# Kernel tuning notes

Measured on AMD Instinct MI355X. Metric: run time of the kernel, lower is better.

The kernel has to match this reference:

```python
import jax, jax.numpy as jnp
import numpy as np


def setup_inputs() -> dict:
    key = jax.random.key(0)
    ks = jax.random.split(key, 7)
    B, S, D = 256, 1024, 128  # batch of sets, set size, n_input
    H = 256
    x = jax.random.normal(ks[0], (B, S, D), dtype=jnp.float32)
    # torch nn.Linear weights: [out_features, in_features], in = 2*layer_in
    W0 = jax.random.normal(ks[1], (H, 2 * D), dtype=jnp.float32) * 0.05
    b0 = jnp.zeros((H,), dtype=jnp.float32)
    W1 = jax.random.normal(ks[2], (H, 2 * H), dtype=jnp.float32) * 0.05
    b1 = jnp.zeros((H,), dtype=jnp.float32)
    W2 = jax.random.normal(ks[3], (H, 2 * H), dtype=jnp.float32) * 0.05
    b2 = jnp.zeros((H,), dtype=jnp.float32)
    return {"x": x, "W0": W0, "b0": b0, "W1": W1, "b1": b1, "W2": W2, "b2": b2}


def reference(x, W0, b0, W1, b1, W2, b2):
    # x: [B, S, D] batch of sets. Original loops over batch; we vmap.
    def apply_set(y):
        # y: [S, d]
        for W, b in ((W0, b0), (W1, b1), (W2, b2)):
            mean = jnp.mean(y, axis=0, keepdims=True)            # [1, d]
            mean = jnp.broadcast_to(mean, y.shape)               # [S, d]
            z = jnp.concatenate([y, mean], axis=1)               # [S, 2d]
            y = jnp.tanh(z @ W.T + b)                            # [S, out]
        return jnp.mean(y, axis=0)                               # [out]
    return jax.vmap(apply_set)(x)                                # [B, out]
```

## Files before the change

### kernel.cpp

```cpp
#include <hip/hip_runtime.h>

#define B_ 256
#define S_ 1024
#define D_ 128
#define H_ 256

typedef short short8 __attribute__((ext_vector_type(8)));
typedef float f32x4 __attribute__((ext_vector_type(4)));

__device__ unsigned short g_Wb0[H_ * D_];
__device__ unsigned short g_Wb1[H_ * H_];
__device__ unsigned short g_Wb2[H_ * H_];
__device__ float g_Wc0[H_ * D_];
__device__ float g_Wc1[H_ * H_];
__device__ float g_Wc2[H_ * H_];
__device__ float g_mean0[B_ * D_];
__device__ float g_colsum1[B_ * H_];
__device__ float g_colsum2[B_ * H_];
__device__ float g_c0[B_ * H_];
__device__ float g_c1[B_ * H_];
__device__ float g_c2[B_ * H_];
__device__ unsigned short g_xb[(size_t)B_ * S_ * D_];

__device__ __forceinline__ unsigned short f2bf(float x) {
    union { float f; unsigned u; } v; v.f = x;
    unsigned r = v.u + 0x7FFFu + ((v.u >> 16) & 1u);
    return (unsigned short)(r >> 16);
}
__device__ __forceinline__ float bf2f(unsigned short h) {
    union { float f; unsigned u; } v; v.u = ((unsigned)h) << 16;
    return v.f;
}
__device__ __forceinline__ float fast_tanh(float x) {
    float e = __builtin_amdgcn_exp2f(x * 2.885390081777927f);
    float r = __builtin_amdgcn_rcpf(1.0f + e);
    return 1.0f - 2.0f * r;
}
__device__ __forceinline__ unsigned cvt_pk_bf16(float lo, float hi) {
    unsigned r;
    asm("v_cvt_pk_bf16_f32 %0, %1, %2" : "=v"(r) : "v"(lo), "v"(hi));
    return r;
}
__device__ __forceinline__ void gload_lds16(const unsigned short* g, unsigned short* l) {
    __builtin_amdgcn_global_load_lds(
        (const __attribute__((address_space(1))) void*)g,
        (__attribute__((address_space(3))) void*)l, 16, 0, 0);
}
__device__ __forceinline__ float row16_reduce_add(float v) {
    int s;
    s = __builtin_amdgcn_update_dpp(0, __builtin_bit_cast(int, v), 0x111, 0xF, 0xF, true);
    v += __builtin_bit_cast(float, s);
    s = __builtin_amdgcn_update_dpp(0, __builtin_bit_cast(int, v), 0x112, 0xF, 0xF, true);
    v += __builtin_bit_cast(float, s);
    s = __builtin_amdgcn_update_dpp(0, __builtin_bit_cast(int, v), 0x114, 0xF, 0xF, true);
    v += __builtin_bit_cast(float, s);
    s = __builtin_amdgcn_update_dpp(0, __builtin_bit_cast(int, v), 0x118, 0xF, 0xF, true);
    v += __builtin_bit_cast(float, s);
    return v;
}

__global__ __launch_bounds__(256) void prep_kernel(
    const float* __restrict__ W0, const float* __restrict__ W1,
    const float* __restrict__ W2)
{
    int i = blockIdx.x * 256 + threadIdx.x;
    const float* W; unsigned short* wb; float* wc; int kbits;
    if (i < H_ * D_) { W = W0; wb = g_Wb0; wc = g_Wc0; kbits = 7; }
    else {
        i -= H_ * D_;
        if (i < H_ * H_) { W = W1; wb = g_Wb1; wc = g_Wc1; kbits = 8; }
        else {
            i -= H_ * H_;
            if (i >= H_ * H_) return;
            W = W2; wb = g_Wb2; wc = g_Wc2; kbits = 8;
        }
    }
    const int K = 1 << kbits, KS = K >> 5;
    const int n = i >> kbits, k = i & (K - 1);
    const float a = W[n * 2 * K + k];
    const float b = W[n * 2 * K + K + k];
    const unsigned short hb = f2bf(a);
    const int w = n >> 5, cf = (n >> 4) & 1, l15 = n & 15;
    const int ks = k >> 5, quad = (k >> 3) & 3, e = k & 7;
    wb[(((w * 2 + cf) * KS + ks) * 64 + quad * 16 + l15) * 8 + e] = hb;
    wc[n * K + k] = b + (a - bf2f(hb));
}

__global__ __launch_bounds__(1024) void means0_kernel(const float* __restrict__ x)
{
    const int set = blockIdx.x, t = threadIdx.x;
    const int cg = t & 31, rg = t >> 5;
    const float* xs = x + (size_t)set * S_ * D_;
    unsigned short* xd = g_xb + (size_t)set * S_ * D_;
    const int slot = cg >> 1, halfsel = (cg & 1) * 4;
    f32x4 s = (f32x4){0.f, 0.f, 0.f, 0.f};
    #pragma unroll 8
    for (int i = 0; i < 32; ++i) {
        const int row = rg + i * 32;
        f32x4 v = *(const f32x4*)(xs + row * D_ + cg * 4);
        s += v;
        uint2 pv;
        pv.x = cvt_pk_bf16(v[0], v[1]);
        pv.y = cvt_pk_bf16(v[2], v[3]);
        *(uint2*)(&xd[row * D_ + ((slot ^ (row & 7)) * 8) + halfsel]) = pv;
    }
    __shared__ f32x4 red[32][32];
    red[rg][cg] = s;
    __syncthreads();
    if (t < 32) {
        f32x4 a = red[0][t];
        #pragma unroll
        for (int g = 1; g < 32; ++g) a += red[g][t];
        #pragma unroll
        for (int c = 0; c < 4; ++c) g_mean0[set * D_ + t * 4 + c] = a[c];
    }
}

template <int L>
__global__ __launch_bounds__(256) void c_kernel(const float* __restrict__ bias)
{
    constexpr int K = (L == 0) ? D_ : H_;
    constexpr int KB = (L == 0) ? 7 : 8;
    const int j = threadIdx.x, sg = blockIdx.x * 4;
    const float* Wc = (L == 0) ? g_Wc0 : (L == 1) ? g_Wc1 : g_Wc2;
    const float* ms = (L == 0) ? g_mean0 : (L == 1) ? g_colsum1 : g_colsum2;
    float* dst = (L == 0) ? g_c0 : (L == 1) ? g_c1 : g_c2;
    __shared__ float m_lds[4][H_];
    for (int i = j; i < 4 * K; i += 256)
        m_lds[i >> KB][i & (K - 1)] = ms[(sg + (i >> KB)) * K + (i & (K - 1))] * (1.f / S_);
    __syncthreads();
    const float* wr = Wc + j * K;
    float a0 = 0.f, a1 = 0.f, a2 = 0.f, a3 = 0.f;
    #pragma unroll 4
    for (int k = 0; k < K; k += 4) {
        f32x4 w = *(const f32x4*)(wr + k);
        #pragma unroll
        for (int c = 0; c < 4; ++c) {
            a0 += m_lds[0][k + c] * w[c];
            a1 += m_lds[1][k + c] * w[c];
            a2 += m_lds[2][k + c] * w[c];
            a3 += m_lds[3][k + c] * w[c];
        }
    }
    const float bb = bias[j];
    dst[(sg + 0) * H_ + j] = bb + a0;
    dst[(sg + 1) * H_ + j] = bb + a1;
    dst[(sg + 2) * H_ + j] = bb + a2;
    dst[(sg + 3) * H_ + j] = bb + a3;
}

template <int LAYER>
__global__ __launch_bounds__(512, 2) void layer_kernel(
    unsigned short* ybuf, float* __restrict__ out)
{
    constexpr int K  = (LAYER == 0) ? D_ : H_;
    constexpr int KS = K / 32;
    constexpr int NCH = (64 * K / 8) / 512;
    constexpr int NT = S_ / 64;
    const int set = blockIdx.x;
    const int t = threadIdx.x;
    const int lane = t & 63, wave = t >> 6;
    const int l15 = lane & 15, quad = lane >> 4;

    __shared__ __align__(16) unsigned short y_lds[2][64 * K];

    const unsigned short* Wb = (LAYER == 0) ? g_Wb0 : (LAYER == 1) ? g_Wb1 : g_Wb2;
    const float* cvec = (LAYER == 0) ? g_c0 : (LAYER == 1) ? g_c1 : g_c2;
    const unsigned short* ysrc = (LAYER == 0) ? g_xb + (size_t)set * S_ * D_
                                              : ybuf + (size_t)set * S_ * H_;
    unsigned short* ydst = ybuf + (size_t)set * S_ * H_;

    short8 wf[2][KS];
    {
        const unsigned short* wb = Wb + (wave * 2 * KS * 64 + lane) * 8;
        #pragma unroll
        for (int cf = 0; cf < 2; ++cf)
            #pragma unroll
            for (int ks = 0; ks < KS; ++ks)
                wf[cf][ks] = *(const short8*)(wb + (cf * KS + ks) * 512);
    }
    const float* cv = cvec + set * H_ + wave * 32 + quad * 4;
    f32x4 creg0 = *(const f32x4*)(cv);
    f32x4 creg1 = *(const f32x4*)(cv + 16);

    #pragma unroll
    for (int c = 0; c < NCH; ++c)
        gload_lds16(ysrc + (c * 512 + t) * 8, &y_lds[0][(c * 512 + t) * 8]);

    f32x4 cs0 = (f32x4){0.f, 0.f, 0.f, 0.f};
    f32x4 cs1 = (f32x4){0.f, 0.f, 0.f, 0.f};
    __syncthreads();

    for (int tt = 0; tt < NT; ++tt) {
        const int buf = tt & 1;
        if (tt + 1 < NT) {
            const unsigned short* src = ysrc + (tt + 1) * 64 * K;
            #pragma unroll
            for (int c = 0; c < NCH; ++c)
                gload_lds16(src + (c * 512 + t) * 8, &y_lds[buf ^ 1][(c * 512 + t) * 8]);
        }
        const unsigned short* yl = y_lds[buf];
        #pragma unroll
        for (int rf = 0; rf < 4; ++rf) {
            short8 bfr[KS];
            #pragma unroll
            for (int ks = 0; ks < KS; ++ks)
                bfr[ks] = *(const short8*)(
                    &yl[(rf * 16 + l15) * K + (((ks * 4 + quad) ^ (l15 & 7)) * 8)]);
            f32x4 ac0 = (f32x4){0.f, 0.f, 0.f, 0.f};
            f32x4 ac1 = (f32x4){0.f, 0.f, 0.f, 0.f};
            #pragma unroll
            for (int ks = 0; ks < KS; ++ks) {
                ac0 = __builtin_amdgcn_mfma_f32_16x16x32_bf16(wf[0][ks], bfr[ks], ac0, 0, 0, 0);
                ac1 = __builtin_amdgcn_mfma_f32_16x16x32_bf16(wf[1][ks], bfr[ks], ac1, 0, 0, 0);
            }
            const int row = tt * 64 + rf * 16 + l15;
            f32x4 th0, th1;
            #pragma unroll
            for (int r = 0; r < 4; ++r) th0[r] = fast_tanh(ac0[r] + creg0[r]);
            #pragma unroll
            for (int r = 0; r < 4; ++r) th1[r] = fast_tanh(ac1[r] + creg1[r]);
            cs0 += th0; cs1 += th1;
            if (LAYER < 2) {
                const int slot0 = wave * 4 + (quad >> 1);
                const int slot1 = slot0 + 2;
                uint2 p0, p1;
                p0.x = cvt_pk_bf16(th0[0], th0[1]); p0.y = cvt_pk_bf16(th0[2], th0[3]);
                p1.x = cvt_pk_bf16(th1[0], th1[1]); p1.y = cvt_pk_bf16(th1[2], th1[3]);
                unsigned short* yr = ydst + row * H_ + (quad & 1) * 4;
                *(uint2*)(&yr[(slot0 ^ (row & 7)) * 8]) = p0;
                *(uint2*)(&yr[(slot1 ^ (row & 7)) * 8]) = p1;
            }
        }
        __syncthreads();
    }

    #pragma unroll
    for (int r = 0; r < 4; ++r) {
        cs0[r] = row16_reduce_add(cs0[r]);
        cs1[r] = row16_reduce_add(cs1[r]);
    }
    if (l15 == 15) {
        const int col = wave * 32 + quad * 4;
        if (LAYER == 2) {
            f32x4 o0, o1;
            #pragma unroll
            for (int r = 0; r < 4; ++r) { o0[r] = cs0[r] * (1.f / S_); o1[r] = cs1[r] * (1.f / S_); }
            *(f32x4*)(&out[set * H_ + col]) = o0;
            *(f32x4*)(&out[set * H_ + col + 16]) = o1;
        } else if (LAYER == 1) {
            *(f32x4*)(&g_colsum2[set * H_ + col]) = cs0;
            *(f32x4*)(&g_colsum2[set * H_ + col + 16]) = cs1;
        } else {
            *(f32x4*)(&g_colsum1[set * H_ + col]) = cs0;
            *(f32x4*)(&g_colsum1[set * H_ + col + 16]) = cs1;
        }
    }
}

extern "C" void kernel_launch(void* const* d_in, const int* in_sizes, int n_in,
                              void* d_out, int out_size, void* d_ws, size_t ws_size,
                              hipStream_t stream) {
    (void)in_sizes; (void)n_in; (void)out_size; (void)ws_size;
    const float* x  = (const float*)d_in[0];
    const float* W0 = (const float*)d_in[1];
    const float* b0 = (const float*)d_in[2];
    const float* W1 = (const float*)d_in[3];
    const float* b1 = (const float*)d_in[4];
    const float* W2 = (const float*)d_in[5];
    const float* b2 = (const float*)d_in[6];
    float* out = (float*)d_out;
    unsigned short* ws = (unsigned short*)d_ws;

    prep_kernel<<<dim3(640), dim3(256), 0, stream>>>(W0, W1, W2);
    means0_kernel<<<dim3(256), dim3(1024), 0, stream>>>(x);
    c_kernel<0><<<dim3(64), dim3(256), 0, stream>>>(b0);
    layer_kernel<0><<<dim3(256), dim3(512), 0, stream>>>(ws, out);
    c_kernel<1><<<dim3(64), dim3(256), 0, stream>>>(b1);
    layer_kernel<1><<<dim3(256), dim3(512), 0, stream>>>(ws, out);
    c_kernel<2><<<dim3(64), dim3(256), 0, stream>>>(b2);
    layer_kernel<2><<<dim3(256), dim3(512), 0, stream>>>(ws, out);
}
```

Measured before the change: 384.6 us.

## Split each set across two blocks with atomic column sums; fuse layer-0 c into means

```diff
diff --git a/kernel.cpp b/kernel.cpp
--- a/kernel.cpp
+++ b/kernel.cpp
@@ -14,7 +14,6 @@
 __device__ float g_Wc0[H_ * D_];
 __device__ float g_Wc1[H_ * H_];
 __device__ float g_Wc2[H_ * H_];
-__device__ float g_mean0[B_ * D_];
 __device__ float g_colsum1[B_ * H_];
 __device__ float g_colsum2[B_ * H_];
 __device__ float g_c0[B_ * H_];
@@ -61,7 +60,7 @@
 
 __global__ __launch_bounds__(256) void prep_kernel(
     const float* __restrict__ W0, const float* __restrict__ W1,
-    const float* __restrict__ W2)
+    const float* __restrict__ W2, float* __restrict__ out)
 {
     int i = blockIdx.x * 256 + threadIdx.x;
     const float* W; unsigned short* wb; float* wc; int kbits;
@@ -71,8 +70,16 @@
         if (i < H_ * H_) { W = W1; wb = g_Wb1; wc = g_Wc1; kbits = 8; }
         else {
             i -= H_ * H_;
-            if (i >= H_ * H_) return;
-            W = W2; wb = g_Wb2; wc = g_Wc2; kbits = 8;
+            if (i < H_ * H_) { W = W2; wb = g_Wb2; wc = g_Wc2; kbits = 8; }
+            else {
+                i -= H_ * H_;
+                if (i < B_ * H_) { g_colsum1[i] = 0.f; return; }
+                i -= B_ * H_;
+                if (i < B_ * H_) { g_colsum2[i] = 0.f; return; }
+                i -= B_ * H_;
+                if (i < B_ * H_) { out[i] = 0.f; }
+                return;
+            }
         }
     }
     const int K = 1 << kbits, KS = K >> 5;
@@ -86,7 +93,8 @@
     wc[n * K + k] = b + (a - bf2f(hb));
 }
 
-__global__ __launch_bounds__(1024) void means0_kernel(const float* __restrict__ x)
+__global__ __launch_bounds__(1024) void means0_kernel(
+    const float* __restrict__ x, const float* __restrict__ b0)
 {
     const int set = blockIdx.x, t = threadIdx.x;
     const int cg = t & 31, rg = t >> 5;
@@ -105,6 +113,7 @@
         *(uint2*)(&xd[row * D_ + ((slot ^ (row & 7)) * 8) + halfsel]) = pv;
     }
     __shared__ f32x4 red[32][32];
+    __shared__ float m_lds[D_];
     red[rg][cg] = s;
     __syncthreads();
     if (t < 32) {
@@ -112,27 +121,37 @@
         #pragma unroll
         for (int g = 1; g < 32; ++g) a += red[g][t];
         #pragma unroll
-        for (int c = 0; c < 4; ++c) g_mean0[set * D_ + t * 4 + c] = a[c];
+        for (int c = 0; c < 4; ++c) m_lds[t * 4 + c] = a[c] * (1.f / S_);
+    }
+    __syncthreads();
+    if (t < H_) {
+        const float* wr = g_Wc0 + t * D_;
+        float acc = 0.f;
+        #pragma unroll 4
+        for (int k = 0; k < D_; k += 4) {
+            f32x4 w = *(const f32x4*)(wr + k);
+            #pragma unroll
+            for (int c = 0; c < 4; ++c) acc += m_lds[k + c] * w[c];
+        }
+        g_c0[set * H_ + t] = b0[t] + acc;
     }
 }
 
 template <int L>
 __global__ __launch_bounds__(256) void c_kernel(const float* __restrict__ bias)
 {
-    constexpr int K = (L == 0) ? D_ : H_;
-    constexpr int KB = (L == 0) ? 7 : 8;
     const int j = threadIdx.x, sg = blockIdx.x * 4;
-    const float* Wc = (L == 0) ? g_Wc0 : (L == 1) ? g_Wc1 : g_Wc2;
-    const float* ms = (L == 0) ? g_mean0 : (L == 1) ? g_colsum1 : g_colsum2;
-    float* dst = (L == 0) ? g_c0 : (L == 1) ? g_c1 : g_c2;
+    const float* Wc = (L == 1) ? g_Wc1 : g_Wc2;
+    const float* ms = (L == 1) ? g_colsum1 : g_colsum2;
+    float* dst = (L == 1) ? g_c1 : g_c2;
     __shared__ float m_lds[4][H_];
-    for (int i = j; i < 4 * K; i += 256)
-        m_lds[i >> KB][i & (K - 1)] = ms[(sg + (i >> KB)) * K + (i & (K - 1))] * (1.f / S_);
+    for (int i = j; i < 4 * H_; i += 256)
+        m_lds[i >> 8][i & (H_ - 1)] = ms[(sg + (i >> 8)) * H_ + (i & (H_ - 1))] * (1.f / S_);
     __syncthreads();
-    const float* wr = Wc + j * K;
+    const float* wr = Wc + j * H_;
     float a0 = 0.f, a1 = 0.f, a2 = 0.f, a3 = 0.f;
     #pragma unroll 4
-    for (int k = 0; k < K; k += 4) {
+    for (int k = 0; k < H_; k += 4) {
         f32x4 w = *(const f32x4*)(wr + k);
         #pragma unroll
         for (int c = 0; c < 4; ++c) {
@@ -150,14 +169,15 @@
 }
 
 template <int LAYER>
-__global__ __launch_bounds__(512, 2) void layer_kernel(
+__global__ __launch_bounds__(512, 4) void layer_kernel(
     unsigned short* ybuf, float* __restrict__ out)
 {
     constexpr int K  = (LAYER == 0) ? D_ : H_;
     constexpr int KS = K / 32;
     constexpr int NCH = (64 * K / 8) / 512;
-    constexpr int NT = S_ / 64;
-    const int set = blockIdx.x;
+    constexpr int NT = 8;
+    const int set = blockIdx.x >> 1;
+    const int rh  = blockIdx.x & 1;
     const int t = threadIdx.x;
     const int lane = t & 63, wave = t >> 6;
     const int l15 = lane & 15, quad = lane >> 4;
@@ -166,9 +186,10 @@
 
     const unsigned short* Wb = (LAYER == 0) ? g_Wb0 : (LAYER == 1) ? g_Wb1 : g_Wb2;
     const float* cvec = (LAYER == 0) ? g_c0 : (LAYER == 1) ? g_c1 : g_c2;
-    const unsigned short* ysrc = (LAYER == 0) ? g_xb + (size_t)set * S_ * D_
-                                              : ybuf + (size_t)set * S_ * H_;
-    unsigned short* ydst = ybuf + (size_t)set * S_ * H_;
+    const unsigned short* ysrc = (LAYER == 0)
+        ? g_xb + ((size_t)set * S_ + rh * 512) * D_
+        : ybuf + ((size_t)set * S_ + rh * 512) * H_;
+    unsigned short* ydst = ybuf + ((size_t)set * S_ + rh * 512) * H_;
 
     short8 wf[2][KS];
     {
@@ -214,7 +235,7 @@
                 ac0 = __builtin_amdgcn_mfma_f32_16x16x32_bf16(wf[0][ks], bfr[ks], ac0, 0, 0, 0);
                 ac1 = __builtin_amdgcn_mfma_f32_16x16x32_bf16(wf[1][ks], bfr[ks], ac1, 0, 0, 0);
             }
-            const int row = tt * 64 + rf * 16 + l15;
+            const int lr = tt * 64 + rf * 16 + l15;
             f32x4 th0, th1;
             #pragma unroll
             for (int r = 0; r < 4; ++r) th0[r] = fast_tanh(ac0[r] + creg0[r]);
@@ -227,9 +248,9 @@
                 uint2 p0, p1;
                 p0.x = cvt_pk_bf16(th0[0], th0[1]); p0.y = cvt_pk_bf16(th0[2], th0[3]);
                 p1.x = cvt_pk_bf16(th1[0], th1[1]); p1.y = cvt_pk_bf16(th1[2], th1[3]);
-                unsigned short* yr = ydst + row * H_ + (quad & 1) * 4;
-                *(uint2*)(&yr[(slot0 ^ (row & 7)) * 8]) = p0;
-                *(uint2*)(&yr[(slot1 ^ (row & 7)) * 8]) = p1;
+                unsigned short* yr = ydst + lr * H_ + (quad & 1) * 4;
+                *(uint2*)(&yr[(slot0 ^ (lr & 7)) * 8]) = p0;
+                *(uint2*)(&yr[(slot1 ^ (lr & 7)) * 8]) = p1;
             }
         }
         __syncthreads();
@@ -243,17 +264,23 @@
     if (l15 == 15) {
         const int col = wave * 32 + quad * 4;
         if (LAYER == 2) {
-            f32x4 o0, o1;
-            #pragma unroll
-            for (int r = 0; r < 4; ++r) { o0[r] = cs0[r] * (1.f / S_); o1[r] = cs1[r] * (1.f / S_); }
-            *(f32x4*)(&out[set * H_ + col]) = o0;
-            *(f32x4*)(&out[set * H_ + col + 16]) = o1;
+            #pragma unroll
+            for (int r = 0; r < 4; ++r) {
+                atomicAdd(&out[set * H_ + col + r],      cs0[r] * (1.f / S_));
+                atomicAdd(&out[set * H_ + col + 16 + r], cs1[r] * (1.f / S_));
+            }
         } else if (LAYER == 1) {
-            *(f32x4*)(&g_colsum2[set * H_ + col]) = cs0;
-            *(f32x4*)(&g_colsum2[set * H_ + col + 16]) = cs1;
+            #pragma unroll
+            for (int r = 0; r < 4; ++r) {
+                atomicAdd(&g_colsum2[set * H_ + col + r],      cs0[r]);
+                atomicAdd(&g_colsum2[set * H_ + col + 16 + r], cs1[r]);
+            }
         } else {
-            *(f32x4*)(&g_colsum1[set * H_ + col]) = cs0;
-            *(f32x4*)(&g_colsum1[set * H_ + col + 16]) = cs1;
+            #pragma unroll
+            for (int r = 0; r < 4; ++r) {
+                atomicAdd(&g_colsum1[set * H_ + col + r],      cs0[r]);
+                atomicAdd(&g_colsum1[set * H_ + col + 16 + r], cs1[r]);
+            }
         }
     }
 }
@@ -272,12 +299,11 @@
     float* out = (float*)d_out;
     unsigned short* ws = (unsigned short*)d_ws;
 
-    prep_kernel<<<dim3(640), dim3(256), 0, stream>>>(W0, W1, W2);
-    means0_kernel<<<dim3(256), dim3(1024), 0, stream>>>(x);
-    c_kernel<0><<<dim3(64), dim3(256), 0, stream>>>(b0);
-    layer_kernel<0><<<dim3(256), dim3(512), 0, stream>>>(ws, out);
+    prep_kernel<<<dim3(1408), dim3(256), 0, stream>>>(W0, W1, W2, out);
+    means0_kernel<<<dim3(256), dim3(1024), 0, stream>>>(x, b0);
+    layer_kernel<0><<<dim3(512), dim3(512), 0, stream>>>(ws, out);
     c_kernel<1><<<dim3(64), dim3(256), 0, stream>>>(b1);
-    layer_kernel<1><<<dim3(256), dim3(512), 0, stream>>>(ws, out);
+    layer_kernel<1><<<dim3(512), dim3(512), 0, stream>>>(ws, out);
     c_kernel<2><<<dim3(64), dim3(256), 0, stream>>>(b2);
-    layer_kernel<2><<<dim3(256), dim3(512), 0, stream>>>(ws, out);
-}
+    layer_kernel<2><<<dim3(512), dim3(512), 0, stream>>>(ws, out);
+}
```

Result: slower. 412.4 us (+7.3%).
